# Optimization experiments

Hardware: AMD Instinct MI355X
Metric: run time of the kernel (lower is better)

Reference implementation:

```python
import jax, jax.numpy as jnp
import numpy as np

N_NODES = 100000
N_EDGES = 1600000
IN_DIM = 256
OUT_DIM = 64


def setup_inputs() -> dict:
    key = jax.random.key(0)
    k1, k2, k3, k4, k5 = jax.random.split(key, 5)
    x = jax.random.normal(k1, (N_NODES, IN_DIM), dtype=jnp.float32)
    # glorot-ish small scales to keep the learned power exponent well-behaved
    W = jax.random.normal(k2, (IN_DIM, OUT_DIM), dtype=jnp.float32) * 0.05
    f_w = jax.random.normal(k3, (2 * OUT_DIM, 1), dtype=jnp.float32) * 0.05
    f_b = jnp.full((1,), 0.5, dtype=jnp.float32)  # constants([1], 0.5)
    row = jax.random.randint(k4, (N_EDGES,), 0, N_NODES, dtype=jnp.int64)
    col = jax.random.randint(k5, (N_EDGES,), 0, N_NODES, dtype=jnp.int64)
    return {"x": x, "W": W, "f_w": f_w, "f_b": f_b, "row": row, "col": col}


def reference(x, W, f_w, f_b, row, col):
    n = x.shape[0]
    pre_sup = x @ W                                   # [N, out]
    vi = pre_sup[row]                                 # [E, out] gather src
    vj = pre_sup[col]                                 # [E, out] gather dst
    # tiny edge MLP: score per edge
    s = jnp.concatenate([vi, vj], axis=1) @ f_w + f_b  # [E, 1]
    # degree = adjacency row-sum including self-loop (adj + I)
    deg = jax.ops.segment_sum(jnp.ones(row.shape[0], x.dtype), row,
                              num_segments=n) + 1.0    # [N]
    deg_vivj = (deg[row] * deg[col])[:, None]          # [E, 1]
    vals = jnp.power(deg_vivj, -s)[:, 0]               # [E] edge weights
    # sparse(support) @ pre_sup  ==  scatter-add over destination rows
    out = jax.ops.segment_sum(vals[:, None] * vj, row, num_segments=n)
    return jax.nn.relu(out)
```

## Files before the change

kernel.cpp:

```cpp
#include <hip/hip_runtime.h>

#define IN_DIM 256
#define OUT_DIM 64

typedef __attribute__((ext_vector_type(8))) short short8;
typedef __attribute__((ext_vector_type(4))) float frag_cd;

__device__ __forceinline__ unsigned short bf16_rne(float f) {
    unsigned u = __float_as_uint(f);
    u = (u + 0x7FFFu + ((u >> 16) & 1u)) >> 16;
    return (unsigned short)u;
}
__device__ __forceinline__ float bf16_to_f32(unsigned short h) {
    return __uint_as_float((unsigned)h << 16);
}

__global__ __launch_bounds__(256) void wprep_kernel(const float* __restrict__ W,
                                                    const float* __restrict__ f_w,
                                                    short8* __restrict__ wfrag,
                                                    float* __restrict__ wf0,
                                                    float* __restrict__ wf1) {
    const int t = threadIdx.x;
    float s0 = 0.f, s1 = 0.f;
    #pragma unroll 8
    for (int c = 0; c < 64; c++) {
        const float w = W[t * 64 + c];
        s0 += w * f_w[c];
        s1 += w * f_w[64 + c];
    }
    wf0[t] = s0;
    wf1[t] = s1;
    for (int e = t; e < 2048; e += 256) {
        const int lane = e & 63;
        const int ct = e >> 6;
        const int chunk = ct >> 2, tile = ct & 3;
        const int kb = chunk * 32 + ((lane >> 4) * 8);
        const int n = tile * 16 + (lane & 15);
        short8 f;
        #pragma unroll
        for (int j = 0; j < 8; j++)
            f[j] = (short)bf16_rne(W[(kb + j) * 64 + n]);
        wfrag[e] = f;
    }
}

__global__ __launch_bounds__(256) void gemm_rank_kernel(const float* __restrict__ x,
                                                        const short8* __restrict__ wfrag,
                                                        const float* __restrict__ wf0,
                                                        const float* __restrict__ wf1,
                                                        unsigned short* __restrict__ pre16,
                                                        float* __restrict__ a,
                                                        float2* __restrict__ bl,
                                                        const int* __restrict__ row,
                                                        unsigned* __restrict__ cnt,
                                                        unsigned* __restrict__ rank,
                                                        int N, int E,
                                                        int nblk_gemm, int nblk_rank) {
    __shared__ short8 lds_wfrag[2048];
    __shared__ float4 lds_wf0[64];
    __shared__ float4 lds_wf1[64];
    const int s = blockIdx.x / 5;
    const int r5 = blockIdx.x % 5;
    if (r5 != 4) {
        const int rb = s * 4 + r5;
        if (rb >= nblk_rank) return;
        const int i = rb * 256 + threadIdx.x;
        if (i < E) {
            const unsigned rk = atomicAdd(&cnt[row[i]], 1u);
            if (rank) rank[i] = rk;
        }
        return;
    }
    if (s >= nblk_gemm) return;
    const int t = threadIdx.x;
    const int w = t >> 6;
    const int l = t & 63;
    const int m = l & 15;
    const int q = l >> 4;
    const int row0 = s * 64 + w * 16;
    const int arow = row0 + m;
    const int arowc = (arow < N) ? arow : (N - 1);
    const float* xr = x + (size_t)arowc * IN_DIM;

    float4 xv[16];
    #pragma unroll
    for (int c = 0; c < 8; c++) {
        xv[2 * c]     = *(const float4*)&xr[c * 32 + q * 8];
        xv[2 * c + 1] = *(const float4*)&xr[c * 32 + q * 8 + 4];
    }
    #pragma unroll
    for (int e = t; e < 2048; e += 256)
        ((int4*)lds_wfrag)[e] = ((const int4*)wfrag)[e];
    if (t < 64) lds_wf0[t] = ((const float4*)wf0)[t];
    else if (t < 128) lds_wf1[t - 64] = ((const float4*)wf1)[t - 64];
    __syncthreads();

    frag_cd acc0 = {0.f, 0.f, 0.f, 0.f};
    frag_cd acc1 = acc0, acc2 = acc0, acc3 = acc0;
    float ap = 0.f, bp = 0.f;

    #pragma unroll
    for (int c = 0; c < 8; c++) {
        const int k4 = c * 8 + q * 2;
        const float4 w0l = lds_wf0[k4];
        const float4 w0h = lds_wf0[k4 + 1];
        const float4 w1l = lds_wf1[k4];
        const float4 w1h = lds_wf1[k4 + 1];
        const short8 b0 = lds_wfrag[(c * 4 + 0) * 64 + l];
        const short8 b1 = lds_wfrag[(c * 4 + 1) * 64 + l];
        const short8 b2 = lds_wfrag[(c * 4 + 2) * 64 + l];
        const short8 b3 = lds_wfrag[(c * 4 + 3) * 64 + l];
        const float4 xl = xv[2 * c];
        const float4 xh = xv[2 * c + 1];

        ap += xl.x * w0l.x + xl.y * w0l.y + xl.z * w0l.z + xl.w * w0l.w
            + xh.x * w0h.x + xh.y * w0h.y + xh.z * w0h.z + xh.w * w0h.w;
        bp += xl.x * w1l.x + xl.y * w1l.y + xl.z * w1l.z + xl.w * w1l.w
            + xh.x * w1h.x + xh.y * w1h.y + xh.z * w1h.z + xh.w * w1h.w;

        short8 a8;
        a8[0] = (short)bf16_rne(xl.x); a8[1] = (short)bf16_rne(xl.y);
        a8[2] = (short)bf16_rne(xl.z); a8[3] = (short)bf16_rne(xl.w);
        a8[4] = (short)bf16_rne(xh.x); a8[5] = (short)bf16_rne(xh.y);
        a8[6] = (short)bf16_rne(xh.z); a8[7] = (short)bf16_rne(xh.w);

        acc0 = __builtin_amdgcn_mfma_f32_16x16x32_bf16(a8, b0, acc0, 0, 0, 0);
        acc1 = __builtin_amdgcn_mfma_f32_16x16x32_bf16(a8, b1, acc1, 0, 0, 0);
        acc2 = __builtin_amdgcn_mfma_f32_16x16x32_bf16(a8, b2, acc2, 0, 0, 0);
        acc3 = __builtin_amdgcn_mfma_f32_16x16x32_bf16(a8, b3, acc3, 0, 0, 0);
    }

    ap += __shfl_xor(ap, 16, 64); ap += __shfl_xor(ap, 32, 64);
    bp += __shfl_xor(bp, 16, 64); bp += __shfl_xor(bp, 32, 64);
    if (q == 0 && arow < N) { a[arow] = ap; bl[arow].x = bp; }

    const frag_cd* accs[4] = {&acc0, &acc1, &acc2, &acc3};
    #pragma unroll
    for (int tt = 0; tt < 4; tt++) {
        #pragma unroll
        for (int r = 0; r < 4; r++) {
            const int ro = row0 + q * 4 + r;
            if (ro < N)
                pre16[(size_t)ro * OUT_DIM + tt * 16 + m] = bf16_rne((*accs[tt])[r]);
        }
    }
}

__global__ __launch_bounds__(256) void scan1_kernel(const unsigned* __restrict__ cnt,
                                                    unsigned* __restrict__ incl,
                                                    unsigned* __restrict__ bsum, int N) {
    __shared__ unsigned s[256];
    const int t = threadIdx.x;
    const int i = blockIdx.x * 256 + t;
    const unsigned v = (i < N) ? cnt[i] : 0u;
    s[t] = v; __syncthreads();
    for (int off = 1; off < 256; off <<= 1) {
        const unsigned u = (t >= off) ? s[t - off] : 0u;
        __syncthreads();
        s[t] += u;
        __syncthreads();
    }
    if (i < N) incl[i] = s[t];
    if (t == 255) bsum[blockIdx.x] = s[255];
}

__global__ __launch_bounds__(512) void scan2_kernel(const unsigned* __restrict__ bsum,
                                                    unsigned* __restrict__ bsum_ex, int nb) {
    __shared__ unsigned s[512];
    const int t = threadIdx.x;
    const unsigned v = (t < nb) ? bsum[t] : 0u;
    s[t] = v; __syncthreads();
    for (int off = 1; off < 512; off <<= 1) {
        const unsigned u = (t >= off) ? s[t - off] : 0u;
        __syncthreads();
        s[t] += u;
        __syncthreads();
    }
    if (t < nb) bsum_ex[t] = s[t] - v;
}

__global__ __launch_bounds__(256) void scan3_kernel(unsigned* __restrict__ row_start,
                                                    const unsigned* __restrict__ cnt,
                                                    float2* __restrict__ bl,
                                                    const unsigned* __restrict__ bsum_ex,
                                                    int N, int E) {
    const int i = blockIdx.x * 256 + threadIdx.x;
    if (i >= N) return;
    const unsigned incl = row_start[i];
    const unsigned c = cnt[i];
    row_start[i] = bsum_ex[blockIdx.x] + incl - c;
    bl[i].y = __logf((float)(c + 1u));
    if (i == N - 1) row_start[N] = (unsigned)E;
}

__global__ __launch_bounds__(256) void scatter_pos_kernel(const int* __restrict__ row,
                                                          const int* __restrict__ col,
                                                          const unsigned* __restrict__ rank,
                                                          const unsigned* __restrict__ row_start,
                                                          int* __restrict__ scol, int E) {
    const int e = blockIdx.x * blockDim.x + threadIdx.x;
    if (e < E)
        scol[row_start[row[e]] + rank[e]] = col[e];
}

__global__ __launch_bounds__(256) void accum_kernel(const unsigned short* __restrict__ pre16,
                                                    const int* __restrict__ scol,
                                                    const unsigned* __restrict__ row_start,
                                                    const float* __restrict__ a,
                                                    const float2* __restrict__ bl,
                                                    const float* __restrict__ f_b,
                                                    float* __restrict__ out, int N) {
    const int lane = threadIdx.x & 63;
    const int eo = lane >> 5;
    const int d = lane & 31;
    const int n = (int)((blockIdx.x * blockDim.x + threadIdx.x) >> 6);
    if (n >= N) return;
    const unsigned* __restrict__ pre32 = (const unsigned*)pre16;
    const unsigned s0 = row_start[n], s1 = row_start[n + 1];
    const float an = a[n] + f_b[0];
    const float ldr = bl[n].y;
    float accx = 0.f, accy = 0.f;
    unsigned j = s0;
    for (; j + 4 <= s1; j += 4) {
        const int c0 = scol[j + eo];
        const int c1 = scol[j + 2 + eo];
        const float2 o0 = bl[c0];
        const float2 o1 = bl[c1];
        const unsigned p0 = pre32[(size_t)c0 * 32 + d];
        const unsigned p1 = pre32[(size_t)c1 * 32 + d];
        const float v0 = __expf(-(an + o0.x) * (ldr + o0.y));
        const float v1 = __expf(-(an + o1.x) * (ldr + o1.y));
        accx += v0 * bf16_to_f32((unsigned short)(p0 & 0xffffu));
        accy += v0 * bf16_to_f32((unsigned short)(p0 >> 16));
        accx += v1 * bf16_to_f32((unsigned short)(p1 & 0xffffu));
        accy += v1 * bf16_to_f32((unsigned short)(p1 >> 16));
    }
    if (j + 2 <= s1) {
        const int c0 = scol[j + eo];
        const float2 o0 = bl[c0];
        const unsigned p0 = pre32[(size_t)c0 * 32 + d];
        const float v0 = __expf(-(an + o0.x) * (ldr + o0.y));
        accx += v0 * bf16_to_f32((unsigned short)(p0 & 0xffffu));
        accy += v0 * bf16_to_f32((unsigned short)(p0 >> 16));
        j += 2;
    }
    if (j < s1 && eo == 0) {
        const int c0 = scol[j];
        const float2 o0 = bl[c0];
        const unsigned p0 = pre32[(size_t)c0 * 32 + d];
        const float v0 = __expf(-(an + o0.x) * (ldr + o0.y));
        accx += v0 * bf16_to_f32((unsigned short)(p0 & 0xffffu));
        accy += v0 * bf16_to_f32((unsigned short)(p0 >> 16));
    }
    accx += __shfl_xor(accx, 32, 64);
    accy += __shfl_xor(accy, 32, 64);
    if (eo == 0) {
        const float2 o = make_float2(fmaxf(accx, 0.f), fmaxf(accy, 0.f));
        *(float2*)&out[(size_t)n * 64 + 2 * d] = o;
    }
}

__global__ __launch_bounds__(256) void edge_atomic_kernel(const unsigned short* __restrict__ pre16,
                                                          const float* __restrict__ a,
                                                          const float2* __restrict__ bl,
                                                          const float* __restrict__ f_b,
                                                          const int* __restrict__ row,
                                                          const int* __restrict__ col,
                                                          float* __restrict__ out, int E) {
    const int lane = threadIdx.x & 63;
    const int wave = (int)((blockIdx.x * blockDim.x + threadIdx.x) >> 6);
    const int nwaves = (int)((gridDim.x * blockDim.x) >> 6);
    const float fb = f_b[0];
    for (int e = wave; e < E; e += nwaves) {
        const int r = row[e];
        const int c = col[e];
        const float s = a[r] + bl[c].x + fb;
        const float val = __expf(-s * (bl[r].y + bl[c].y));
        atomicAdd(&out[(size_t)r * 64 + lane],
                  val * bf16_to_f32(pre16[(size_t)c * 64 + lane]));
    }
}

__global__ __launch_bounds__(256) void relu_kernel(float4* __restrict__ out, int n4) {
    const int i = blockIdx.x * blockDim.x + threadIdx.x;
    if (i < n4) {
        float4 v = out[i];
        v.x = fmaxf(v.x, 0.f); v.y = fmaxf(v.y, 0.f);
        v.z = fmaxf(v.z, 0.f); v.w = fmaxf(v.w, 0.f);
        out[i] = v;
    }
}

extern "C" void kernel_launch(void* const* d_in, const int* in_sizes, int n_in,
                              void* d_out, int out_size, void* d_ws, size_t ws_size,
                              hipStream_t stream) {
    const float* x   = (const float*)d_in[0];
    const float* W   = (const float*)d_in[1];
    const float* f_w = (const float*)d_in[2];
    const float* f_b = (const float*)d_in[3];
    const int*   row = (const int*)d_in[4];
    const int*   col = (const int*)d_in[5];
    float* out = (float*)d_out;

    const int N = in_sizes[0] / IN_DIM;
    const int E = in_sizes[4];

    size_t off = 0;
    auto salloc = [&](size_t bytes) { size_t p = off; off = (off + bytes + 255) & ~(size_t)255; return p; };
    char* w8 = (char*)d_ws;
    unsigned short* pre16 = (unsigned short*)(w8 + salloc((size_t)N * OUT_DIM * sizeof(unsigned short)));
    unsigned* row_start = (unsigned*)(w8 + salloc((size_t)(N + 1) * sizeof(unsigned)));
    unsigned* cnt       = (unsigned*)(w8 + salloc((size_t)N * sizeof(unsigned)));
    float*    a         = (float*)   (w8 + salloc((size_t)N * sizeof(float)));
    float2*   bl        = (float2*)  (w8 + salloc((size_t)N * sizeof(float2)));
    unsigned* bsum      = (unsigned*)(w8 + salloc(512 * sizeof(unsigned)));
    unsigned* bsum_ex   = (unsigned*)(w8 + salloc(512 * sizeof(unsigned)));
    short8*   wfrag     = (short8*)  (w8 + salloc(2048 * sizeof(short8)));
    float*    wf0       = (float*)   (w8 + salloc(256 * sizeof(float)));
    float*    wf1       = (float*)   (w8 + salloc(256 * sizeof(float)));
    int*      scol      = (int*)     (w8 + salloc((size_t)E * sizeof(int)));
    unsigned* rank      = (unsigned*)(w8 + salloc((size_t)E * sizeof(unsigned)));
    const size_t need_full = off;

    const int nb = (N + 255) / 256;
    const int nblk_gemm = (N + 63) / 64;
    const int nblk_node = (N + 3) / 4;
    const int nblk_edge = (E + 255) / 256;
    const int stripes = (((nblk_edge + 3) / 4) > nblk_gemm) ? ((nblk_edge + 3) / 4) : nblk_gemm;
    const int nblk_fused = stripes * 5;

    hipMemsetAsync(cnt, 0, (size_t)N * sizeof(unsigned), stream);
    wprep_kernel<<<1, 256, 0, stream>>>(W, f_w, wfrag, wf0, wf1);

    if (need_full <= ws_size) {
        gemm_rank_kernel<<<nblk_fused, 256, 0, stream>>>(x, wfrag, wf0, wf1, pre16, a, bl,
                                                         row, cnt, rank, N, E,
                                                         nblk_gemm, nblk_edge);
        scan1_kernel<<<nb, 256, 0, stream>>>(cnt, row_start, bsum, N);
        scan2_kernel<<<1, 512, 0, stream>>>(bsum, bsum_ex, nb);
        scan3_kernel<<<nb, 256, 0, stream>>>(row_start, cnt, bl, bsum_ex, N, E);
        scatter_pos_kernel<<<nblk_edge, 256, 0, stream>>>(row, col, rank, row_start, scol, E);
        accum_kernel<<<nblk_node, 256, 0, stream>>>(pre16, scol, row_start, a, bl, f_b, out, N);
    } else {
        gemm_rank_kernel<<<nblk_fused, 256, 0, stream>>>(x, wfrag, wf0, wf1, pre16, a, bl,
                                                         row, cnt, (unsigned*)nullptr, N, E,
                                                         nblk_gemm, nblk_edge);
        scan1_kernel<<<nb, 256, 0, stream>>>(cnt, row_start, bsum, N);
        scan2_kernel<<<1, 512, 0, stream>>>(bsum, bsum_ex, nb);
        scan3_kernel<<<nb, 256, 0, stream>>>(row_start, cnt, bl, bsum_ex, N, E);
        hipMemsetAsync(out, 0, (size_t)out_size * sizeof(float), stream);
        edge_atomic_kernel<<<4096, 256, 0, stream>>>(pre16, a, bl, f_b, row, col, out, E);
        const int n4 = out_size / 4;
        relu_kernel<<<(n4 + 255) / 256, 256, 0, stream>>>((float4*)out, n4);
    }
}
```

Measured before the change: 322.0 us.

## Persistent GEMM tiles, batch rank atomics, drop scan2 kernel, unroll accumulation by eight

The fused GEMM/rank kernel changes shape. GEMM blocks become persistent, capped at 512 and striding over tiles, and each rank block now issues four edge atomics per thread. The second scan kernel is removed: each scan3 block instead reduces the preceding block sums itself. The accumulation loop gains an 8-edge unrolled path to expose more memory-level parallelism. Together these aim to cut launch count and the number of blocks, at the cost of redundant prefix reductions in scan3 and possibly less latency hiding in the persistent GEMM.

```diff
diff --git a/kernel.cpp b/kernel.cpp
--- a/kernel.cpp
+++ b/kernel.cpp
@@ -55,39 +55,39 @@
                                                         unsigned* __restrict__ cnt,
                                                         unsigned* __restrict__ rank,
                                                         int N, int E,
-                                                        int nblk_gemm, int nblk_rank) {
+                                                        int nblk_gemm, int nblk_rank, int G) {
     __shared__ short8 lds_wfrag[2048];
     __shared__ float4 lds_wf0[64];
     __shared__ float4 lds_wf1[64];
-    const int s = blockIdx.x / 5;
-    const int r5 = blockIdx.x % 5;
-    if (r5 != 4) {
-        const int rb = s * 4 + r5;
+    const int r4 = blockIdx.x & 3;
+    const int s = blockIdx.x >> 2;
+    if (r4 != 3) {
+        const int rb = s * 3 + r4;
         if (rb >= nblk_rank) return;
-        const int i = rb * 256 + threadIdx.x;
-        if (i < E) {
-            const unsigned rk = atomicAdd(&cnt[row[i]], 1u);
-            if (rank) rank[i] = rk;
+        const int i0 = rb * 1024 + threadIdx.x;
+        const int i1 = i0 + 256, i2 = i0 + 512, i3 = i0 + 768;
+        const bool v0 = i0 < E, v1 = i1 < E, v2 = i2 < E, v3 = i3 < E;
+        unsigned rk0 = 0, rk1 = 0, rk2 = 0, rk3 = 0;
+        if (v0) rk0 = atomicAdd(&cnt[row[i0]], 1u);
+        if (v1) rk1 = atomicAdd(&cnt[row[i1]], 1u);
+        if (v2) rk2 = atomicAdd(&cnt[row[i2]], 1u);
+        if (v3) rk3 = atomicAdd(&cnt[row[i3]], 1u);
+        if (rank) {
+            if (v0) rank[i0] = rk0;
+            if (v1) rank[i1] = rk1;
+            if (v2) rank[i2] = rk2;
+            if (v3) rank[i3] = rk3;
         }
         return;
     }
-    if (s >= nblk_gemm) return;
+    const int g = s;
+    if (g >= G) return;
     const int t = threadIdx.x;
     const int w = t >> 6;
     const int l = t & 63;
     const int m = l & 15;
     const int q = l >> 4;
-    const int row0 = s * 64 + w * 16;
-    const int arow = row0 + m;
-    const int arowc = (arow < N) ? arow : (N - 1);
-    const float* xr = x + (size_t)arowc * IN_DIM;
-
-    float4 xv[16];
-    #pragma unroll
-    for (int c = 0; c < 8; c++) {
-        xv[2 * c]     = *(const float4*)&xr[c * 32 + q * 8];
-        xv[2 * c + 1] = *(const float4*)&xr[c * 32 + q * 8 + 4];
-    }
+
     #pragma unroll
     for (int e = t; e < 2048; e += 256)
         ((int4*)lds_wfrag)[e] = ((const int4*)wfrag)[e];
@@ -95,53 +95,68 @@
     else if (t < 128) lds_wf1[t - 64] = ((const float4*)wf1)[t - 64];
     __syncthreads();
 
-    frag_cd acc0 = {0.f, 0.f, 0.f, 0.f};
-    frag_cd acc1 = acc0, acc2 = acc0, acc3 = acc0;
-    float ap = 0.f, bp = 0.f;
-
-    #pragma unroll
-    for (int c = 0; c < 8; c++) {
-        const int k4 = c * 8 + q * 2;
-        const float4 w0l = lds_wf0[k4];
-        const float4 w0h = lds_wf0[k4 + 1];
-        const float4 w1l = lds_wf1[k4];
-        const float4 w1h = lds_wf1[k4 + 1];
-        const short8 b0 = lds_wfrag[(c * 4 + 0) * 64 + l];
-        const short8 b1 = lds_wfrag[(c * 4 + 1) * 64 + l];
-        const short8 b2 = lds_wfrag[(c * 4 + 2) * 64 + l];
-        const short8 b3 = lds_wfrag[(c * 4 + 3) * 64 + l];
-        const float4 xl = xv[2 * c];
-        const float4 xh = xv[2 * c + 1];
-
-        ap += xl.x * w0l.x + xl.y * w0l.y + xl.z * w0l.z + xl.w * w0l.w
-            + xh.x * w0h.x + xh.y * w0h.y + xh.z * w0h.z + xh.w * w0h.w;
-        bp += xl.x * w1l.x + xl.y * w1l.y + xl.z * w1l.z + xl.w * w1l.w
-            + xh.x * w1h.x + xh.y * w1h.y + xh.z * w1h.z + xh.w * w1h.w;
-
-        short8 a8;
-        a8[0] = (short)bf16_rne(xl.x); a8[1] = (short)bf16_rne(xl.y);
-        a8[2] = (short)bf16_rne(xl.z); a8[3] = (short)bf16_rne(xl.w);
-        a8[4] = (short)bf16_rne(xh.x); a8[5] = (short)bf16_rne(xh.y);
-        a8[6] = (short)bf16_rne(xh.z); a8[7] = (short)bf16_rne(xh.w);
-
-        acc0 = __builtin_amdgcn_mfma_f32_16x16x32_bf16(a8, b0, acc0, 0, 0, 0);
-        acc1 = __builtin_amdgcn_mfma_f32_16x16x32_bf16(a8, b1, acc1, 0, 0, 0);
-        acc2 = __builtin_amdgcn_mfma_f32_16x16x32_bf16(a8, b2, acc2, 0, 0, 0);
-        acc3 = __builtin_amdgcn_mfma_f32_16x16x32_bf16(a8, b3, acc3, 0, 0, 0);
-    }
-
-    ap += __shfl_xor(ap, 16, 64); ap += __shfl_xor(ap, 32, 64);
-    bp += __shfl_xor(bp, 16, 64); bp += __shfl_xor(bp, 32, 64);
-    if (q == 0 && arow < N) { a[arow] = ap; bl[arow].x = bp; }
-
-    const frag_cd* accs[4] = {&acc0, &acc1, &acc2, &acc3};
-    #pragma unroll
-    for (int tt = 0; tt < 4; tt++) {
+    for (int tile = g; tile < nblk_gemm; tile += G) {
+        const int row0 = tile * 64 + w * 16;
+        const int arow = row0 + m;
+        const int arowc = (arow < N) ? arow : (N - 1);
+        const float* xr = x + (size_t)arowc * IN_DIM;
+
+        float4 xv[16];
         #pragma unroll
-        for (int r = 0; r < 4; r++) {
-            const int ro = row0 + q * 4 + r;
-            if (ro < N)
-                pre16[(size_t)ro * OUT_DIM + tt * 16 + m] = bf16_rne((*accs[tt])[r]);
+        for (int c = 0; c < 8; c++) {
+            xv[2 * c]     = *(const float4*)&xr[c * 32 + q * 8];
+            xv[2 * c + 1] = *(const float4*)&xr[c * 32 + q * 8 + 4];
+        }
+        __builtin_amdgcn_sched_barrier(0);
+
+        frag_cd acc0 = {0.f, 0.f, 0.f, 0.f};
+        frag_cd acc1 = acc0, acc2 = acc0, acc3 = acc0;
+        float ap = 0.f, bp = 0.f;
+
+        #pragma unroll
+        for (int c = 0; c < 8; c++) {
+            const int k4 = c * 8 + q * 2;
+            const float4 w0l = lds_wf0[k4];
+            const float4 w0h = lds_wf0[k4 + 1];
+            const float4 w1l = lds_wf1[k4];
+            const float4 w1h = lds_wf1[k4 + 1];
+            const short8 b0 = lds_wfrag[(c * 4 + 0) * 64 + l];
+            const short8 b1 = lds_wfrag[(c * 4 + 1) * 64 + l];
+            const short8 b2 = lds_wfrag[(c * 4 + 2) * 64 + l];
+            const short8 b3 = lds_wfrag[(c * 4 + 3) * 64 + l];
+            const float4 xl = xv[2 * c];
+            const float4 xh = xv[2 * c + 1];
+
+            ap += xl.x * w0l.x + xl.y * w0l.y + xl.z * w0l.z + xl.w * w0l.w
+                + xh.x * w0h.x + xh.y * w0h.y + xh.z * w0h.z + xh.w * w0h.w;
+            bp += xl.x * w1l.x + xl.y * w1l.y + xl.z * w1l.z + xl.w * w1l.w
+                + xh.x * w1h.x + xh.y * w1h.y + xh.z * w1h.z + xh.w * w1h.w;
+
+            short8 a8;
+            a8[0] = (short)bf16_rne(xl.x); a8[1] = (short)bf16_rne(xl.y);
+            a8[2] = (short)bf16_rne(xl.z); a8[3] = (short)bf16_rne(xl.w);
+            a8[4] = (short)bf16_rne(xh.x); a8[5] = (short)bf16_rne(xh.y);
+            a8[6] = (short)bf16_rne(xh.z); a8[7] = (short)bf16_rne(xh.w);
+
+            acc0 = __builtin_amdgcn_mfma_f32_16x16x32_bf16(a8, b0, acc0, 0, 0, 0);
+            acc1 = __builtin_amdgcn_mfma_f32_16x16x32_bf16(a8, b1, acc1, 0, 0, 0);
+            acc2 = __builtin_amdgcn_mfma_f32_16x16x32_bf16(a8, b2, acc2, 0, 0, 0);
+            acc3 = __builtin_amdgcn_mfma_f32_16x16x32_bf16(a8, b3, acc3, 0, 0, 0);
+        }
+
+        ap += __shfl_xor(ap, 16, 64); ap += __shfl_xor(ap, 32, 64);
+        bp += __shfl_xor(bp, 16, 64); bp += __shfl_xor(bp, 32, 64);
+        if (q == 0 && arow < N) { a[arow] = ap; bl[arow].x = bp; }
+
+        const frag_cd* accs[4] = {&acc0, &acc1, &acc2, &acc3};
+        #pragma unroll
+        for (int tt = 0; tt < 4; tt++) {
+            #pragma unroll
+            for (int r = 0; r < 4; r++) {
+                const int ro = row0 + q * 4 + r;
+                if (ro < N)
+                    pre16[(size_t)ro * OUT_DIM + tt * 16 + m] = bf16_rne((*accs[tt])[r]);
+            }
         }
     }
 }
@@ -164,31 +179,27 @@
     if (t == 255) bsum[blockIdx.x] = s[255];
 }
 
-__global__ __launch_bounds__(512) void scan2_kernel(const unsigned* __restrict__ bsum,
-                                                    unsigned* __restrict__ bsum_ex, int nb) {
-    __shared__ unsigned s[512];
-    const int t = threadIdx.x;
-    const unsigned v = (t < nb) ? bsum[t] : 0u;
-    s[t] = v; __syncthreads();
-    for (int off = 1; off < 512; off <<= 1) {
-        const unsigned u = (t >= off) ? s[t - off] : 0u;
-        __syncthreads();
-        s[t] += u;
-        __syncthreads();
-    }
-    if (t < nb) bsum_ex[t] = s[t] - v;
-}
-
 __global__ __launch_bounds__(256) void scan3_kernel(unsigned* __restrict__ row_start,
                                                     const unsigned* __restrict__ cnt,
                                                     float2* __restrict__ bl,
-                                                    const unsigned* __restrict__ bsum_ex,
+                                                    const unsigned* __restrict__ bsum,
                                                     int N, int E) {
-    const int i = blockIdx.x * 256 + threadIdx.x;
+    __shared__ unsigned red[256];
+    const int t = threadIdx.x;
+    unsigned partial = 0;
+    for (int k = t; k < (int)blockIdx.x; k += 256) partial += bsum[k];
+    red[t] = partial; __syncthreads();
+    #pragma unroll
+    for (int off = 128; off > 0; off >>= 1) {
+        if (t < off) red[t] += red[t + off];
+        __syncthreads();
+    }
+    const unsigned ex0 = red[0];
+    const int i = blockIdx.x * 256 + t;
     if (i >= N) return;
     const unsigned incl = row_start[i];
     const unsigned c = cnt[i];
-    row_start[i] = bsum_ex[blockIdx.x] + incl - c;
+    row_start[i] = ex0 + incl - c;
     bl[i].y = __logf((float)(c + 1u));
     if (i == N - 1) row_start[N] = (unsigned)E;
 }
@@ -221,6 +232,32 @@
     const float ldr = bl[n].y;
     float accx = 0.f, accy = 0.f;
     unsigned j = s0;
+    for (; j + 8 <= s1; j += 8) {
+        const int c0 = scol[j + eo];
+        const int c1 = scol[j + 2 + eo];
+        const int c2 = scol[j + 4 + eo];
+        const int c3 = scol[j + 6 + eo];
+        const float2 o0 = bl[c0];
+        const float2 o1 = bl[c1];
+        const float2 o2 = bl[c2];
+        const float2 o3 = bl[c3];
+        const unsigned p0 = pre32[(size_t)c0 * 32 + d];
+        const unsigned p1 = pre32[(size_t)c1 * 32 + d];
+        const unsigned p2 = pre32[(size_t)c2 * 32 + d];
+        const unsigned p3 = pre32[(size_t)c3 * 32 + d];
+        const float v0 = __expf(-(an + o0.x) * (ldr + o0.y));
+        const float v1 = __expf(-(an + o1.x) * (ldr + o1.y));
+        const float v2 = __expf(-(an + o2.x) * (ldr + o2.y));
+        const float v3 = __expf(-(an + o3.x) * (ldr + o3.y));
+        accx += v0 * bf16_to_f32((unsigned short)(p0 & 0xffffu));
+        accy += v0 * bf16_to_f32((unsigned short)(p0 >> 16));
+        accx += v1 * bf16_to_f32((unsigned short)(p1 & 0xffffu));
+        accy += v1 * bf16_to_f32((unsigned short)(p1 >> 16));
+        accx += v2 * bf16_to_f32((unsigned short)(p2 & 0xffffu));
+        accy += v2 * bf16_to_f32((unsigned short)(p2 >> 16));
+        accx += v3 * bf16_to_f32((unsigned short)(p3 & 0xffffu));
+        accy += v3 * bf16_to_f32((unsigned short)(p3 >> 16));
+    }
     for (; j + 4 <= s1; j += 4) {
         const int c0 = scol[j + eo];
         const int c1 = scol[j + 2 + eo];
@@ -314,7 +351,6 @@
     float*    a         = (float*)   (w8 + salloc((size_t)N * sizeof(float)));
     float2*   bl        = (float2*)  (w8 + salloc((size_t)N * sizeof(float2)));
     unsigned* bsum      = (unsigned*)(w8 + salloc(512 * sizeof(unsigned)));
-    unsigned* bsum_ex   = (unsigned*)(w8 + salloc(512 * sizeof(unsigned)));
     short8*   wfrag     = (short8*)  (w8 + salloc(2048 * sizeof(short8)));
     float*    wf0       = (float*)   (w8 + salloc(256 * sizeof(float)));
     float*    wf1       = (float*)   (w8 + salloc(256 * sizeof(float)));
@@ -326,8 +362,10 @@
     const int nblk_gemm = (N + 63) / 64;
     const int nblk_node = (N + 3) / 4;
     const int nblk_edge = (E + 255) / 256;
-    const int stripes = (((nblk_edge + 3) / 4) > nblk_gemm) ? ((nblk_edge + 3) / 4) : nblk_gemm;
-    const int nblk_fused = stripes * 5;
+    const int nblk_rank = (E + 1023) / 1024;
+    const int G = (nblk_gemm < 512) ? nblk_gemm : 512;
+    const int stripes = (((nblk_rank + 2) / 3) > G) ? ((nblk_rank + 2) / 3) : G;
+    const int nblk_fused = stripes * 4;
 
     hipMemsetAsync(cnt, 0, (size_t)N * sizeof(unsigned), stream);
     wprep_kernel<<<1, 256, 0, stream>>>(W, f_w, wfrag, wf0, wf1);
@@ -335,19 +373,17 @@
     if (need_full <= ws_size) {
         gemm_rank_kernel<<<nblk_fused, 256, 0, stream>>>(x, wfrag, wf0, wf1, pre16, a, bl,
                                                          row, cnt, rank, N, E,
-                                                         nblk_gemm, nblk_edge);
+                                                         nblk_gemm, nblk_rank, G);
         scan1_kernel<<<nb, 256, 0, stream>>>(cnt, row_start, bsum, N);
-        scan2_kernel<<<1, 512, 0, stream>>>(bsum, bsum_ex, nb);
-        scan3_kernel<<<nb, 256, 0, stream>>>(row_start, cnt, bl, bsum_ex, N, E);
+        scan3_kernel<<<nb, 256, 0, stream>>>(row_start, cnt, bl, bsum, N, E);
         scatter_pos_kernel<<<nblk_edge, 256, 0, stream>>>(row, col, rank, row_start, scol, E);
         accum_kernel<<<nblk_node, 256, 0, stream>>>(pre16, scol, row_start, a, bl, f_b, out, N);
     } else {
         gemm_rank_kernel<<<nblk_fused, 256, 0, stream>>>(x, wfrag, wf0, wf1, pre16, a, bl,
                                                          row, cnt, (unsigned*)nullptr, N, E,
-                                                         nblk_gemm, nblk_edge);
+                                                         nblk_gemm, nblk_rank, G);
         scan1_kernel<<<nb, 256, 0, stream>>>(cnt, row_start, bsum, N);
-        scan2_kernel<<<1, 512, 0, stream>>>(bsum, bsum_ex, nb);
-        scan3_kernel<<<nb, 256, 0, stream>>>(row_start, cnt, bl, bsum_ex, N, E);
+        scan3_kernel<<<nb, 256, 0, stream>>>(row_start, cnt, bl, bsum, N, E);
         hipMemsetAsync(out, 0, (size_t)out_size * sizeof(float), stream);
         edge_atomic_kernel<<<4096, 256, 0, stream>>>(pre16, a, bl, f_b, row, col, out, E);
         const int n4 = out_size / 4;
```

Result: slower. 342.0 us (+6.2%).
